# Kernel tuning notes

Hardware: AMD Instinct MI355X
Metric: run time of the kernel (lower is better)

The kernel has to match this reference:

```python
import jax, jax.numpy as jnp
import numpy as np


def _shift(x, k):
    # roll time axis forward by k, zero-filling the first k steps
    if k == 0:
        return x
    return jnp.pad(x, ((0, 0), (k, 0), (0, 0)))[:, : x.shape[1]]


def _stu_conv(u, v, n):
    # u: (B,L,D), v: (L,K) spectral filters; non-tensordot branch of conv()
    B, L, D = u.shape
    K = v.shape[1]
    sgn = jnp.where(jnp.arange(L) % 2 == 1, -1.0, 1.0).astype(jnp.float32)[None, :, None, None]
    ue = jnp.broadcast_to(u[:, :, None, :], (B, L, K, D)).astype(jnp.float32)
    U = jnp.stack([ue, ue * sgn], axis=-1)                     # (B,L,K,D,2)
    Uf = jnp.fft.rfft(U, n=n, axis=1)
    vf = jnp.fft.rfft(v.astype(jnp.float32)[None, :, :, None, None], n=n, axis=1)
    Uc = jnp.fft.irfft(vf * Uf, n=n, axis=1)[:, :L]            # (B,L,K,D,2)
    U_plus = Uc[..., 0]
    U_minus = Uc[..., 1] * sgn
    return U_plus.astype(u.dtype), U_minus.astype(u.dtype)


def setup_inputs() -> dict:
    key = jax.random.key(0)
    ks = jax.random.split(key, 6)
    B, L, D, K, k_u, k_y = 2, 1024, 512, 16, 3, 2
    u = jax.random.normal(ks[0], (B, L, D), jnp.float32)
    filters = jax.random.normal(ks[1], (L, K), jnp.float32) / np.float32(np.sqrt(L))
    M_u = jax.random.normal(ks[2], (D, k_u, D), jnp.float32) * 0.01
    M_y = jax.random.normal(ks[3], (D, k_y, D), jnp.float32) * 0.01
    M_phi_plus = jax.random.normal(ks[4], (K, D, D), jnp.float32) * 0.01
    M_phi_minus = jax.random.normal(ks[5], (K, D, D), jnp.float32) * 0.01
    return {"u": u, "filters": filters, "M_u": M_u, "M_y": M_y,
            "M_phi_plus": M_phi_plus, "M_phi_minus": M_phi_minus}


def reference(u, filters, M_u, M_y, M_phi_plus, M_phi_minus):
    B, L, D = u.shape
    n = 1 << int(np.ceil(np.log2(2 * L - 1)))  # nearest power of two >= 2L-1
    k_u = M_u.shape[1]
    k_y = M_y.shape[1]

    # FFT-based long convolution with the +/- sign trick
    U_plus, U_minus = _stu_conv(u, filters, n)
    spectral = (jnp.einsum('blkd,kdo->blo', U_plus, M_phi_plus)
                + jnp.einsum('blkd,kdo->blo', U_minus, M_phi_minus))

    # input-AR term of compute_ar_strict: sum_j u[t+1-j] @ M_u[:, j-1].T (shifts 0..k_u-1)
    u_sh = jnp.stack([_shift(u, j - 1) for j in range(1, k_u + 1)], axis=1)  # (B,k_u,L,D)
    y_in = jnp.einsum('bjlf,ijf->bli', u_sh, M_u)

    z = spectral + y_in  # (B,L,D)

    # output-AR recurrence of compute_ar_strict as a scan
    def step(y_buf, z_t):
        y_t = z_t + jnp.einsum('bjf,djf->bd', y_buf, M_y)
        y_buf = jnp.concatenate([y_t[:, None], y_buf[:, :-1]], axis=1)
        return y_buf, y_t

    _, ys = jax.lax.scan(step, jnp.zeros((B, k_y, D), z.dtype), jnp.swapaxes(z, 0, 1))
    return jnp.swapaxes(ys, 0, 1)  # (B,L,D)
```

## Files before the change

### kernel.cpp

```cpp
#include <hip/hip_runtime.h>
#include <hip/hip_bf16.h>


using bf16 = __hip_bfloat16;
typedef __attribute__((ext_vector_type(8))) short bf16x8;
typedef __attribute__((ext_vector_type(4))) float f32x4;

#define B_   2
#define L_   1024
#define D_   512
#define K_   16
#define KT   17920
#define ROWS 2048
#define NTAP 6
#define PBLD 3584
#define SPLITD 8
#define SPLITR 6
#define ZBROWS 1032

#define WAIT_VM4 0x0F74
#define WAIT_VM0 0x0F70

__device__ __forceinline__ void gll16(const void* g, void* l) {
    __builtin_amdgcn_global_load_lds(
        (const __attribute__((address_space(1))) unsigned int*)g,
        (__attribute__((address_space(3))) unsigned int*)l, 16, 0, 0);
}

__global__ void prep_all(const float* __restrict__ u, const float* __restrict__ fil,
                         const float* __restrict__ Mu, const float* __restrict__ My,
                         const float* __restrict__ Mp, const float* __restrict__ Mm,
                         bf16* __restrict__ U, bf16* __restrict__ BT,
                         bf16* __restrict__ PB, bf16* __restrict__ W,
                         bf16* __restrict__ Myb, bf16* __restrict__ BTT,
                         bf16* __restrict__ uPT) {
    __shared__ bf16 t[64][72];
    int bid = blockIdx.x, tid = threadIdx.x;
    auto pack4 = [](float4 v) {
        ushort4 o; bf16 h;
        h = __float2bfloat16(v.x); o.x = *(unsigned short*)&h;
        h = __float2bfloat16(v.y); o.y = *(unsigned short*)&h;
        h = __float2bfloat16(v.z); o.z = *(unsigned short*)&h;
        h = __float2bfloat16(v.w); o.w = *(unsigned short*)&h;
        return o;
    };
    if (bid < 3072) {
        int e4 = bid * 256 + tid;
        int r = e4 / 384, rem = e4 % 384;
        int tt = rem >> 7, f = (rem & 127) * 4;
        int b = r >> 10, l = r & 1023;
        float4 v = {0.f, 0.f, 0.f, 0.f};
        if (l >= tt) v = *(const float4*)&u[((size_t)b * L_ + l - tt) * D_ + f];
        *(ushort4*)&U[(size_t)r * KT + 16384 + tt * 512 + f] = pack4(v);
    } else if (bid < 3840) {
        int e4 = (bid - 3072) * 256 + tid;
        int o = e4 / 384, tf4 = (e4 % 384) * 4;
        float4 v = *(const float4*)&Mu[(size_t)o * 1536 + tf4];
        *(ushort4*)&BT[(size_t)o * KT + 16384 + tf4] = pack4(v);
    } else if (bid < 4352) {
        int e4 = (bid - 3840) * 256 + tid;
        int n = e4 >> 8, c4 = (e4 & 255) * 4;
        float4 v;
        if (c4 < 512) {
            v.x = (n == c4) ? 1.f : 0.f;     v.y = (n == c4 + 1) ? 1.f : 0.f;
            v.z = (n == c4 + 2) ? 1.f : 0.f; v.w = (n == c4 + 3) ? 1.f : 0.f;
        } else v = *(const float4*)&My[(size_t)n * 1024 + (c4 - 512)];
        *(ushort4*)&PB[(size_t)n * PBLD + c4] = pack4(v);
    } else if (bid < 5120) {
        int tile = bid - 4352;
        int set = tile >> 8, rem = tile & 255;
        int k = rem >> 4, g = (rem >> 2) & 3, kb = rem & 3;
        for (int idx = tid; idx < 4096; idx += 256) {
            int i = idx >> 5, jp = idx & 31;
            int j = ((jp >> 3) ^ ((i >> 1) & 3)) * 8 + (jp & 7);
            int x = g * 128 + i - kb * 32 - j - (set == 2 ? 1 : 0);
            float v = 0.f;
            if (x >= 0) {
                int row = (set == 0) ? 2 * x : 2 * x + 1;
                v = fil[row * K_ + k];
            }
            W[(size_t)tile * 4096 + idx] = __float2bfloat16(v);
        }
    } else if (bid < 5632) {
        int e4 = (bid - 5120) * 256 + tid;
        float4 v = *(const float4*)&My[(size_t)e4 * 4];
        *(ushort4*)&Myb[(size_t)e4 * 4] = pack4(v);
    } else {
        int tt = bid - 5632;
        int zb = tt >> 6, rem = tt & 63;
        int bx = rem & 7, by = rem >> 3;
        int col = tid & 63, r0 = (tid >> 6) * 16;
        if (zb < 32) {
            int dt = bx * 64, ot = by * 64, c = zb;
            int k = c & 15;
            const float* sp = Mp + (size_t)k * D_ * D_;
            const float* sm = Mm + (size_t)k * D_ * D_;
            float sg = (c < 16) ? 1.f : -1.f;
            for (int i = 0; i < 16; ++i) {
                size_t o_ = (size_t)(dt + r0 + i) * D_ + ot + col;
                t[r0 + i][col] = __float2bfloat16(sp[o_] + sg * sm[o_]);
            }
            __syncthreads();
            for (int i = 0; i < 16; ++i)
                BT[(size_t)(ot + r0 + i) * KT + c * D_ + dt + col] = t[col][r0 + i];
        } else if (zb < 34) {
            int h = zb - 32;
            int dt = bx * 64, ft = by * 64;
            for (int i = 0; i < 16; ++i)
                t[r0 + i][col] = __float2bfloat16(My[(size_t)(dt + r0 + i) * 1024 + (1 - h) * 512 + ft + col]);
            __syncthreads();
            for (int i = 0; i < 16; ++i)
                BTT[(size_t)(ft + r0 + i) * 1024 + h * 512 + dt + col] = t[col][r0 + i];
        } else {
            for (int it = 0; it < 4; ++it) {
                int b = it >> 1, p = it & 1;
                int mt = bx * 64, dt = by * 64;
                __syncthreads();
                for (int i = 0; i < 16; ++i)
                    t[r0 + i][col] = __float2bfloat16(u[((size_t)b * L_ + 2 * (mt + r0 + i) + p) * D_ + dt + col]);
                __syncthreads();
                for (int i = 0; i < 16; ++i)
                    uPT[((size_t)it * 512 + dt + r0 + i) * 512 + mt + col] = t[col][r0 + i];
            }
        }
    }
}

__device__ __forceinline__ void phi_body(
    const bf16* A, int lda, const bf16* BT, int ldb,
    bf16* out, int ldo, int klen, const bf16* add, int lad,
    int row0, int col0, bf16* sA, bf16* sB)
{
    const int tid = threadIdx.x, lane = tid & 63, wave = tid >> 6;
    const int wm = (wave & 1) * 64, wn = (wave >> 1) * 64;
    const int ml = lane & 15, q = lane >> 4;
    const int srow = lane >> 2, scol = (((lane & 3) ^ ((srow >> 1) & 3))) * 8;
    const int swz = ((ml >> 1) & 3);
    f32x4 acc[4][4] = {};

    for (int k = 0; k < klen; k += 32) {
        __syncthreads();
        #pragma unroll
        for (int repi = 0; repi < 2; ++repi) {
            int a = wave + repi * 4;
            gll16(A  + (size_t)(row0 + a * 16 + srow) * lda + k + scol, &sA[a * 512]);
            gll16(BT + (size_t)(col0 + a * 16 + srow) * ldb + k + scol, &sB[a * 512]);
        }
        __syncthreads();
        bf16x8 af[4], bfr[4];
        #pragma unroll
        for (int i = 0; i < 4; ++i)
            af[i] = *(const bf16x8*)&sA[(wm + i * 16 + ml) * 32 + (q ^ swz) * 8];
        #pragma unroll
        for (int j = 0; j < 4; ++j)
            bfr[j] = *(const bf16x8*)&sB[(wn + j * 16 + ml) * 32 + (q ^ swz) * 8];
        #pragma unroll
        for (int i = 0; i < 4; ++i)
            #pragma unroll
            for (int j = 0; j < 4; ++j)
                acc[i][j] = __builtin_amdgcn_mfma_f32_16x16x32_bf16(af[i], bfr[j], acc[i][j], 0, 0, 0);
    }
    #pragma unroll
    for (int i = 0; i < 4; ++i)
        #pragma unroll
        for (int j = 0; j < 4; ++j)
            #pragma unroll
            for (int reg = 0; reg < 4; ++reg) {
                int r = row0 + wm + i * 16 + q * 4 + reg;
                int cc = col0 + wn + j * 16 + ml;
                float v = acc[i][j][reg];
                if (add) v += __bfloat162float(add[(size_t)r * lad + cc]);
                out[(size_t)r * ldo + cc] = __float2bfloat16(v);
            }
}

__global__ void k_ztaps(const bf16* __restrict__ partD, float* __restrict__ z,
                        bf16* __restrict__ zbuf, bf16* PB, const bf16* BTT) {
    __shared__ bf16 sA[4096];
    __shared__ bf16 sB[4096];
    int bid = blockIdx.x;
    if (bid < 32) {
        int row0 = (bid & 3) * 128, col0 = (bid >> 2) * 128;
        phi_body(PB + 3 * 512, PBLD, BTT, 1024, PB + 5 * 512, PBLD, 1024,
                 nullptr, 0, row0, col0, sA, sB);
        return;
    }
    if (bid == 32) {
        ushort4 z4 = {0, 0, 0, 0};
        for (int i = 0; i < 8; ++i) {
            int e4 = i * 256 + threadIdx.x;
            int b = e4 >> 10, rem = e4 & 1023;
            int g = rem >> 7, c4 = (rem & 127) * 4;
            *(ushort4*)&zbuf[(size_t)(b * ZBROWS + g) * 512 + c4] = z4;
        }
        return;
    }
    int t = (bid - 33) * 256 + threadIdx.x;
    int r = t >> 7, f4 = (t & 127) * 4;
    const ushort4* p = (const ushort4*)partD;
    float4 s = {0.f, 0.f, 0.f, 0.f};
    #pragma unroll
    for (int c = 0; c < SPLITD; ++c) {
        ushort4 v = p[(size_t)c * (ROWS * D_ / 4) + t];
        s.x += __uint_as_float((unsigned)v.x << 16);
        s.y += __uint_as_float((unsigned)v.y << 16);
        s.z += __uint_as_float((unsigned)v.z << 16);
        s.w += __uint_as_float((unsigned)v.w << 16);
    }
    ((float4*)z)[t] = s;
    ushort4 zb4;
    { bf16 h;
      h = __float2bfloat16(s.x); zb4.x = *(unsigned short*)&h;
      h = __float2bfloat16(s.y); zb4.y = *(unsigned short*)&h;
      h = __float2bfloat16(s.z); zb4.z = *(unsigned short*)&h;
      h = __float2bfloat16(s.w); zb4.w = *(unsigned short*)&h; }
    int b = r >> 10, li = r & 1023;
    *(ushort4*)&zbuf[(size_t)(b * ZBROWS + 8 + li) * 512 + f4] = zb4;
}

__global__ void reduce_out(const float* __restrict__ z, const bf16* __restrict__ partR,
                           float* __restrict__ out) {
    int t = blockIdx.x * 256 + threadIdx.x;
    if (t >= ROWS * D_ / 4) return;
    float4 s = ((const float4*)z)[t];
    const ushort4* p = (const ushort4*)partR;
    #pragma unroll
    for (int c = 0; c < SPLITR; ++c) {
        ushort4 v = p[(size_t)c * (ROWS * D_ / 4) + t];
        s.x += __uint_as_float((unsigned)v.x << 16);
        s.y += __uint_as_float((unsigned)v.y << 16);
        s.z += __uint_as_float((unsigned)v.z << 16);
        s.w += __uint_as_float((unsigned)v.w << 16);
    }
    ((float4*)out)[t] = s;
}

__global__ __launch_bounds__(256, 3) void conv_misc(
    const bf16* __restrict__ W, const bf16* __restrict__ uPT,
    bf16* __restrict__ U,
    const bf16* PB, const bf16* BTT, const bf16* Myb)
{
    __shared__ bf16 sA[3][4096];
    __shared__ bf16 sB[3][4096];
    const int z = blockIdx.z;
    if (z < 3) {
        int row0 = blockIdx.x * 128, col0 = blockIdx.y * 128;
        bf16* BTTw = (bf16*)BTT; bf16* PBw = (bf16*)PB;
        if (z == 0)
            phi_body(PB, PBLD, BTT, 1024, PBw + 2 * 512, PBLD, 1024,
                     nullptr, 0, row0, col0, &sA[0][0], &sB[0][0]);
        else if (z == 1)
            phi_body(BTT + 512, 1024, Myb + 512, 1024,
                     BTTw + (size_t)512 * 1024, 1024, 512,
                     nullptr, 0, row0, col0, &sA[0][0], &sB[0][0]);
        else
            phi_body(BTT + 512, 1024, Myb, 1024,
                     BTTw + (size_t)512 * 1024 + 512, 1024, 512,
                     BTT, 1024, row0, col0, &sA[0][0], &sB[0][0]);
        return;
    }
    const int zc = z - 3;
    const int mt = 3 - blockIdx.x, dt = blockIdx.y * 128;
    const int t = zc & 3, b = (zc >> 2) & 1, k = zc >> 3;
    const int pb_ = t & 1;
    const int p = (t & 1) ^ (t >> 1);
    const int set = (t < 2) ? 0 : (t == 2 ? 1 : 2);
    const int ch = (t < 2) ? k : 16 + k;
    const int plane = b * 2 + pb_;
    const int tid = threadIdx.x, lane = tid & 63, wave = tid >> 6;
    const int wm = (wave & 1) * 64, wn = (wave >> 1) * 64;
    const int ml = lane & 15, q = lane >> 4;
    const int srow = lane >> 2, scol = (((lane & 3) ^ ((srow >> 1) & 3))) * 8;
    const int swz = ((ml >> 1) & 3);
    f32x4 acc[4][4] = {};
    const int n = (mt + 1) * 4;

    const bf16* bB0 = uPT + ((size_t)plane * 512 + dt + wave * 16       + srow) * 512 + scol;
    const bf16* bB1 = uPT + ((size_t)plane * 512 + dt + (wave + 4) * 16 + srow) * 512 + scol;
    const bf16* wbase = W + ((size_t)(set * 16 + k) * 16) * 4096;
    auto stage = [&](int s, int buf) {
        const bf16* wt = wbase + ((size_t)((mt - (s >> 2)) * 4 + (s & 3))) * 4096;
        gll16(wt + wave * 512 + lane * 8, &sA[buf][wave * 512]);
        gll16(wt + (wave + 4) * 512 + lane * 8, &sA[buf][(wave + 4) * 512]);
        gll16(bB0 + s * 32, &sB[buf][wave * 512]);
        gll16(bB1 + s * 32, &sB[buf][(wave + 4) * 512]);
    };
    auto compute = [&](int c) {
        bf16x8 af[4], bfr[4];
        #pragma unroll
        for (int i = 0; i < 4; ++i)
            af[i] = *(const bf16x8*)&sA[c][(wm + i * 16 + ml) * 32 + (q ^ swz) * 8];
        #pragma unroll
        for (int j = 0; j < 4; ++j)
            bfr[j] = *(const bf16x8*)&sB[c][(wn + j * 16 + ml) * 32 + (q ^ swz) * 8];
        #pragma unroll
        for (int i = 0; i < 4; ++i)
            #pragma unroll
            for (int j = 0; j < 4; ++j)
                acc[i][j] = __builtin_amdgcn_mfma_f32_16x16x32_bf16(af[i], bfr[j], acc[i][j], 0, 0, 0);
    };
    stage(0, 0); stage(1, 1);
    int c = 0, nb = 2;
    for (int i = 0; i < n - 1; ++i) {
        __builtin_amdgcn_s_waitcnt(WAIT_VM4);
        __builtin_amdgcn_s_barrier();
        if (i + 2 < n) stage(i + 2, nb);
        compute(c);
        c = (c == 2) ? 0 : c + 1; nb = (nb == 2) ? 0 : nb + 1;
    }
    __builtin_amdgcn_s_waitcnt(WAIT_VM0);
    __builtin_amdgcn_s_barrier();
    compute(c);

    #pragma unroll
    for (int i = 0; i < 4; ++i)
        #pragma unroll
        for (int j = 0; j < 4; ++j)
            #pragma unroll
            for (int reg = 0; reg < 4; ++reg) {
                int m = mt * 128 + wm + i * 16 + q * 4 + reg;
                int l = 2 * m + p;
                int d = dt + wn + j * 16 + ml;
                U[(size_t)(b * L_ + l) * KT + ch * 512 + d] = __float2bfloat16(acc[i][j][reg]);
            }
}

__device__ __forceinline__ void mm128_pair(
    const bf16* Abase, int alda, const bf16* Bbase, int ldb, int n,
    bf16* o, int row0, int col0, bf16 (*sA)[4096], bf16 (*sB)[4096])
{
    const int tid = threadIdx.x, lane = tid & 63, wave = tid >> 6;
    const int wm = (wave & 1) * 64, wn = (wave >> 1) * 64;
    const int ml = lane & 15, q = lane >> 4;
    const int srow = lane >> 2, scol = (((lane & 3) ^ ((srow >> 1) & 3))) * 8;
    const int swz = ((ml >> 1) & 3);
    f32x4 acc[4][4] = {};

    const bf16* bA0 = Abase + (size_t)(wave * 16 + srow) * alda + scol;
    const bf16* bA1 = Abase + (size_t)((wave + 4) * 16 + srow) * alda + scol;
    const bf16* bB0 = Bbase + (size_t)(wave * 16 + srow) * ldb + scol;
    const bf16* bB1 = Bbase + (size_t)((wave + 4) * 16 + srow) * ldb + scol;
    auto stage = [&](int s) {
        int buf = s & 3;
        gll16(bA0 + s * 32, &sA[buf][wave * 512]);
        gll16(bA1 + s * 32, &sA[buf][(wave + 4) * 512]);
        gll16(bB0 + s * 32, &sB[buf][wave * 512]);
        gll16(bB1 + s * 32, &sB[buf][(wave + 4) * 512]);
    };
    auto compute = [&](int c) {
        bf16x8 af[4], bfr[4];
        #pragma unroll
        for (int i = 0; i < 4; ++i)
            af[i] = *(const bf16x8*)&sA[c][(wm + i * 16 + ml) * 32 + (q ^ swz) * 8];
        #pragma unroll
        for (int j = 0; j < 4; ++j)
            bfr[j] = *(const bf16x8*)&sB[c][(wn + j * 16 + ml) * 32 + (q ^ swz) * 8];
        #pragma unroll
        for (int i = 0; i < 4; ++i)
            #pragma unroll
            for (int j = 0; j < 4; ++j)
                acc[i][j] = __builtin_amdgcn_mfma_f32_16x16x32_bf16(af[i], bfr[j], acc[i][j], 0, 0, 0);
    };
    stage(0); stage(1);
    const int npair = n >> 1;
    for (int p = 0; p < npair; ++p) {
        __builtin_amdgcn_s_waitcnt(WAIT_VM0);
        __builtin_amdgcn_s_barrier();
        if (2 * p + 2 < n) { stage(2 * p + 2); stage(2 * p + 3); }
        compute((2 * p) & 3);
        compute((2 * p + 1) & 3);
    }
    #pragma unroll
    for (int i = 0; i < 4; ++i)
        #pragma unroll
        for (int j = 0; j < 4; ++j)
            #pragma unroll
            for (int reg = 0; reg < 4; ++reg) {
                int r = row0 + wm + i * 16 + q * 4 + reg;
                int cc = col0 + wn + j * 16 + ml;
                o[(size_t)r * D_ + cc] = __float2bfloat16(acc[i][j][reg]);
            }
}

__global__ __launch_bounds__(256, 2) void gemm_d(
    const bf16* __restrict__ U, const bf16* __restrict__ BT,
    bf16* __restrict__ part, const bf16* PB, const bf16* BTT)
{
    __shared__ bf16 sA[4][4096];
    __shared__ bf16 sB[4][4096];
    int id = blockIdx.x;
    if (id < 32) {
        int r0_ = (id & 3) * 128, c0_ = (id >> 2) * 128;
        phi_body(PB + 512, PBLD, BTT, 1024, (bf16*)PB + 3 * 512, PBLD, 1024,
                 nullptr, 0, r0_, c0_, &sA[0][0], &sB[0][0]);
        return;
    }
    id -= 32;
    const int xcd = id & 7, n_ = id >> 3;
    const int zz = xcd;
    const int row0 = (n_ >> 2) * 128, col0 = (n_ & 3) * 128;
    const int kc = KT / SPLITD;
    mm128_pair(U + (size_t)row0 * KT + (size_t)zz * kc, KT,
               BT + (size_t)col0 * KT + (size_t)zz * kc, KT,
               kc >> 5, part + (size_t)zz * ROWS * D_, row0, col0, sA, sB);
}

__global__ __launch_bounds__(256, 2) void gemm_r(
    const bf16* __restrict__ zbuf, const bf16* __restrict__ BT,
    bf16* __restrict__ part)
{
    __shared__ bf16 sA[4][4096];
    __shared__ bf16 sB[4][4096];
    const int row0 = blockIdx.x * 128, col0 = blockIdx.y * 128;
    const int zz = blockIdx.z;
    const int s = 1 + zz;
    const int b = row0 >> 10, li0 = row0 & 1023;
    mm128_pair(zbuf + ((size_t)(b * ZBROWS + 8 + li0 - s)) * 512, 512,
               BT + (size_t)col0 * PBLD + (size_t)zz * 512, PBLD,
               16, part + (size_t)zz * ROWS * D_, row0, col0, sA, sB);
}

extern "C" void kernel_launch(void* const* d_in, const int* in_sizes, int n_in,
                              void* d_out, int out_size, void* d_ws, size_t ws_size,
                              hipStream_t stream) {
    const float* u   = (const float*)d_in[0];
    const float* fil = (const float*)d_in[1];
    const float* Mu  = (const float*)d_in[2];
    const float* My  = (const float*)d_in[3];
    const float* Mp  = (const float*)d_in[4];
    const float* Mm  = (const float*)d_in[5];
    float* out = (float*)d_out;

    char* ws = (char*)d_ws;
    size_t off = 0;
    auto alloc = [&](size_t bytes) { void* p = ws + off; off = (off + bytes + 255) & ~(size_t)255; return p; };
    bf16*  U    = (bf16*) alloc((size_t)ROWS * KT * 2);
    bf16*  BT   = (bf16*) alloc((size_t)512 * KT * 2);
    bf16*  PB   = (bf16*) alloc((size_t)512 * PBLD * 2);
    bf16*  BTT  = (bf16*) alloc((size_t)1024 * 1024 * 2);
    bf16*  Myb  = (bf16*) alloc((size_t)512 * 1024 * 2);
    float* z    = (float*)alloc((size_t)ROWS * D_ * 4);
    bf16*  zb   = (bf16*) alloc((size_t)B_ * ZBROWS * 512 * 2);
    char*  region = (char*)alloc((size_t)16 * ROWS * D_ * 2);
    bf16*  W    = (bf16*)region;
    bf16*  uPT  = (bf16*)(region + (size_t)768 * 4096 * 2);
    bf16*  partD = (bf16*)region;
    bf16*  partR = (bf16*)region;

    prep_all<<<7872, 256, 0, stream>>>(u, fil, Mu, My, Mp, Mm,
                                       U, BT, PB, W, Myb, BTT, uPT);

    conv_misc<<<dim3(4, 4, 131), 256, 0, stream>>>(W, uPT, U, PB, BTT, Myb);

    gemm_d<<<544, 256, 0, stream>>>(U, BT, partD, PB, BTT);

    k_ztaps<<<1057, 256, 0, stream>>>(partD, z, zb, PB, BTT);

    gemm_r<<<dim3(16, 4, SPLITR), 256, 0, stream>>>(zb, PB + 512, partR);

    reduce_out<<<(ROWS * D_ / 4 + 255) / 256, 256, 0, stream>>>(z, partR, out);
}
```

Baseline: 258.6 us.

## Rewrite split-K GEMM with 256x256 tiles, 512 threads and triple buffering

The main spectral GEMM now gives each 512-thread block a 256x256 output tile instead of a 128x128 tile per 256-thread block. It uses a 3-buffer LDS pipeline with one k-step per barrier, and the split-K factor rises from 8 to 14 so the grid still fills the device with 224 GEMM blocks plus 32 phi blocks. Larger tiles raise arithmetic intensity and reuse of the A/B operands loaded into LDS. The cost is higher register and LDS use with only one block per CU, and more partial sums for the later reduction to read. The idle upper waves in the phi blocks spin on a fixed count of barriers to match phi_body, which is fragile.

New measurement: 244.9 us. 5.3% less time.

```diff
diff --git a/kernel.cpp b/kernel.cpp
--- a/kernel.cpp
+++ b/kernel.cpp
@@ -14,7 +14,7 @@
 #define ROWS 2048
 #define NTAP 6
 #define PBLD 3584
-#define SPLITD 8
+#define SPLITD 14
 #define SPLITR 6
 #define ZBROWS 1032
 
@@ -325,6 +325,89 @@
             }
 }
 
+__global__ __launch_bounds__(512, 1) void gemm_d(
+    const bf16* __restrict__ U, const bf16* __restrict__ BT,
+    bf16* __restrict__ part, const bf16* PB, const bf16* BTT)
+{
+    __shared__ bf16 sA[3][8192];
+    __shared__ bf16 sB[3][8192];
+    int id = blockIdx.x;
+    const int tid = threadIdx.x, lane = tid & 63, wave = tid >> 6;
+    if (id < 32) {
+        if (wave >= 4) {
+            for (int i = 0; i < 64; ++i) __syncthreads();
+            return;
+        }
+        int r0_ = (id & 3) * 128, c0_ = (id >> 2) * 128;
+        phi_body(PB + 512, PBLD, BTT, 1024, (bf16*)PB + 3 * 512, PBLD, 1024,
+                 nullptr, 0, r0_, c0_, &sA[0][0], &sB[0][0]);
+        return;
+    }
+    id -= 32;
+    const int zz = id >> 4;
+    const int n_ = id & 15;
+    const int row0 = (n_ >> 1) * 256, col0 = (n_ & 1) * 256;
+    const int kc = KT / SPLITD;
+    const int k0 = zz * kc;
+    const int n = kc >> 5;
+
+    const int wm = (wave & 3) * 64, wn = (wave >> 2) * 128;
+    const int ml = lane & 15, q = lane >> 4;
+    const int srow = lane >> 2, scol = (((lane & 3) ^ ((srow >> 1) & 3))) * 8;
+    const int swz = ((ml >> 1) & 3);
+    f32x4 acc[4][8] = {};
+
+    const int a0 = 2 * wave, a1 = 2 * wave + 1;
+    const bf16* bA0 = U  + (size_t)(row0 + a0 * 16 + srow) * KT + k0 + scol;
+    const bf16* bA1 = U  + (size_t)(row0 + a1 * 16 + srow) * KT + k0 + scol;
+    const bf16* bB0 = BT + (size_t)(col0 + a0 * 16 + srow) * KT + k0 + scol;
+    const bf16* bB1 = BT + (size_t)(col0 + a1 * 16 + srow) * KT + k0 + scol;
+    auto stage = [&](int s, int buf) {
+        gll16(bA0 + s * 32, &sA[buf][a0 * 512]);
+        gll16(bA1 + s * 32, &sA[buf][a1 * 512]);
+        gll16(bB0 + s * 32, &sB[buf][a0 * 512]);
+        gll16(bB1 + s * 32, &sB[buf][a1 * 512]);
+    };
+    auto compute = [&](int c) {
+        bf16x8 af[4], bfr[8];
+        #pragma unroll
+        for (int i = 0; i < 4; ++i)
+            af[i] = *(const bf16x8*)&sA[c][(wm + i * 16 + ml) * 32 + (q ^ swz) * 8];
+        #pragma unroll
+        for (int j = 0; j < 8; ++j)
+            bfr[j] = *(const bf16x8*)&sB[c][(wn + j * 16 + ml) * 32 + (q ^ swz) * 8];
+        #pragma unroll
+        for (int i = 0; i < 4; ++i)
+            #pragma unroll
+            for (int j = 0; j < 8; ++j)
+                acc[i][j] = __builtin_amdgcn_mfma_f32_16x16x32_bf16(af[i], bfr[j], acc[i][j], 0, 0, 0);
+    };
+    stage(0, 0); stage(1, 1);
+    int c = 0, nb = 2;
+    for (int i = 0; i < n - 1; ++i) {
+        __builtin_amdgcn_s_waitcnt(WAIT_VM4);
+        __builtin_amdgcn_s_barrier();
+        if (i + 2 < n) stage(i + 2, nb);
+        compute(c);
+        c = (c == 2) ? 0 : c + 1; nb = (nb == 2) ? 0 : nb + 1;
+    }
+    __builtin_amdgcn_s_waitcnt(WAIT_VM0);
+    __builtin_amdgcn_s_barrier();
+    compute(c);
+
+    bf16* o = part + (size_t)zz * ROWS * D_;
+    #pragma unroll
+    for (int i = 0; i < 4; ++i)
+        #pragma unroll
+        for (int j = 0; j < 8; ++j)
+            #pragma unroll
+            for (int reg = 0; reg < 4; ++reg) {
+                int r = row0 + wm + i * 16 + q * 4 + reg;
+                int cc = col0 + wn + j * 16 + ml;
+                o[(size_t)r * D_ + cc] = __float2bfloat16(acc[i][j][reg]);
+            }
+}
+
 __device__ __forceinline__ void mm128_pair(
     const bf16* Abase, int alda, const bf16* Bbase, int ldb, int n,
     bf16* o, int row0, int col0, bf16 (*sA)[4096], bf16 (*sB)[4096])
@@ -380,29 +463,6 @@
                 int cc = col0 + wn + j * 16 + ml;
                 o[(size_t)r * D_ + cc] = __float2bfloat16(acc[i][j][reg]);
             }
-}
-
-__global__ __launch_bounds__(256, 2) void gemm_d(
-    const bf16* __restrict__ U, const bf16* __restrict__ BT,
-    bf16* __restrict__ part, const bf16* PB, const bf16* BTT)
-{
-    __shared__ bf16 sA[4][4096];
-    __shared__ bf16 sB[4][4096];
-    int id = blockIdx.x;
-    if (id < 32) {
-        int r0_ = (id & 3) * 128, c0_ = (id >> 2) * 128;
-        phi_body(PB + 512, PBLD, BTT, 1024, (bf16*)PB + 3 * 512, PBLD, 1024,
-                 nullptr, 0, r0_, c0_, &sA[0][0], &sB[0][0]);
-        return;
-    }
-    id -= 32;
-    const int xcd = id & 7, n_ = id >> 3;
-    const int zz = xcd;
-    const int row0 = (n_ >> 2) * 128, col0 = (n_ & 3) * 128;
-    const int kc = KT / SPLITD;
-    mm128_pair(U + (size_t)row0 * KT + (size_t)zz * kc, KT,
-               BT + (size_t)col0 * KT + (size_t)zz * kc, KT,
-               kc >> 5, part + (size_t)zz * ROWS * D_, row0, col0, sA, sB);
 }
 
 __global__ __launch_bounds__(256, 2) void gemm_r(
@@ -452,7 +512,7 @@
 
     conv_misc<<<dim3(4, 4, 131), 256, 0, stream>>>(W, uPT, U, PB, BTT, Myb);
 
-    gemm_d<<<544, 256, 0, stream>>>(U, BT, partD, PB, BTT);
+    gemm_d<<<256, 512, 0, stream>>>(U, BT, partD, PB, BTT);
 
     k_ztaps<<<1057, 256, 0, stream>>>(partD, z, zb, PB, BTT);
 
```
